# Performance work log

Hardware: AMD Instinct MI355X
Metric: run time of the kernel (lower is better)

Reference implementation:

```python
import jax, jax.numpy as jnp
import numpy as np

N_HEADS = 2
EPS = 1e-5
NEG_SLOPE = 0.02
N_CENTROIDS = 1024
RADII = (0.1, 0.2)
KS = (32, 64)


def fps(x, m):
    # Farthest point sampling (deterministic start at index 0). x: [B, C, N]
    B, C, N = x.shape
    def body(carry, _):
        distance, farthest = carry
        centroid = jnp.take_along_axis(x, jnp.broadcast_to(farthest[:, None, None], (B, C, 1)), axis=2)
        dist = jnp.sum((x - centroid) ** 2, axis=1)  # [B, N]
        distance = jnp.minimum(distance, dist)
        nxt = jnp.argmax(distance, axis=1).astype(jnp.int32)
        return (distance, nxt), farthest
    init = (jnp.full((B, N), 1e10, x.dtype), jnp.zeros((B,), jnp.int32))
    _, idxs = jax.lax.scan(body, init, None, length=m)
    return idxs.T  # [B, m]


def ball_group(x, centroids, radius, k):
    # x: [B, C, N], centroids: [B, C, M] -> (idx [B,M,k] int32, mask [B,M,k] bool)
    B, C, N = x.shape
    M = centroids.shape[2]
    d = (jnp.sum(x * x, axis=1)[:, None, :]
         - 2.0 * jnp.einsum('bcm,bcn->bmn', centroids, x)
         + jnp.sum(centroids * centroids, axis=1)[:, :, None])  # [B, M, N]
    idx = jnp.broadcast_to(jnp.arange(N, dtype=jnp.int32)[None, None, :], (B, M, N))
    idx = jnp.where(d > radius * radius, N, idx)
    idx = -jax.lax.top_k(-idx, k)[0]  # k smallest indices, ascending (matches torch.topk largest=False)
    mask = idx == N
    first = jnp.where(idx[:, :, :1] == N, 0, idx[:, :, :1])
    idx = jnp.where(mask, jnp.broadcast_to(first, idx.shape), idx)
    return idx, mask


def attention_mix(x, y, mask, wq, wk, wv, wo):
    # x: [B, C, K] centroids, y: [B, C, K, Np] groups, mask: [B, K, Np]
    B, C, K = x.shape
    Np = y.shape[3]
    H = N_HEADS
    q = jnp.einsum('oc,bck->bok', wq, x).reshape(B, H, C, K)
    kk = jnp.einsum('oc,bckn->bokn', wk, y).reshape(B, H, C, K, Np)
    v = jnp.einsum('oc,bckn->bokn', wv, y).reshape(B, H, C, K, Np)
    w = jnp.einsum('bhck,bhckn->bhkn', q, kk) / (C ** 0.5)
    w = jnp.where(mask[:, None, :, :], -1e9, w)
    w = jax.nn.softmax(w, axis=3)
    o = jnp.einsum('bhkn,bhckn->bhck', w, v).reshape(B, H * C, K)
    return jnp.einsum('oc,bck->bok', wo, o) + x


def conv_bn(x, w, b, g, beta, act):
    # 1x1 Conv1d + BatchNorm1d (training-mode batch stats) + optional LeakyReLU(0.02)
    x = jnp.einsum('oc,bck->bok', w, x) + b[None, :, None]
    mu = jnp.mean(x, axis=(0, 2), keepdims=True)
    var = jnp.var(x, axis=(0, 2), keepdims=True)
    x = (x - mu) * jax.lax.rsqrt(var + EPS) * g[None, :, None] + beta[None, :, None]
    return jnp.where(x > 0, x, NEG_SLOPE * x) if act else x


def pointnet_msg(xyz, point_features, attn_params, mlp_params):
    support = jnp.concatenate([xyz, point_features], axis=1)  # [B, 32, N]
    B, Cs, N = support.shape
    M = N_CENTROIDS
    cidx = fps(support, M)  # [B, M]
    centroids = jnp.take_along_axis(support, jnp.broadcast_to(cidx[:, None, :], (B, Cs, M)), axis=2)
    new_xyz = jnp.take_along_axis(xyz, jnp.broadcast_to(cidx[:, None, :], (B, 3, M)), axis=2)
    feats = []
    for s, (radius, k) in enumerate(zip(RADII, KS)):
        idx, mask = ball_group(support, centroids, radius, k)  # [B, M, k]
        gidx = jnp.broadcast_to(idx.reshape(B, 1, M * k), (B, Cs, M * k))
        group = jnp.take_along_axis(support, gidx, axis=2).reshape(B, Cs, M, k)
        group = group - centroids[:, :, :, None]
        f = attention_mix(centroids, group, mask, *attn_params[s])
        (w0, b0, g0, t0), (w1, b1, g1, t1) = mlp_params[s]
        f = conv_bn(f, w0, b0, g0, t0, act=True)
        f = conv_bn(f, w1, b1, g1, t1, act=False)
        feats.append(f)
    return new_xyz, jnp.concatenate(feats, axis=1)  # [B,3,M], [B,256,M]


def setup_inputs() -> dict:
    key = jax.random.key(0)
    ks = jax.random.split(key, 32)
    B, N, C = 4, 16384, 32
    d = {}
    d['xyz'] = jax.random.uniform(ks[0], (B, 3, N), jnp.float32)
    d['point_features'] = jax.random.normal(ks[1], (B, C - 3, N), jnp.float32)
    i = 2
    for s in range(2):
        d[f'aq{s}'] = 0.05 * jax.random.normal(ks[i], (64, 32), jnp.float32); i += 1
        d[f'ak{s}'] = 0.05 * jax.random.normal(ks[i], (64, 32), jnp.float32); i += 1
        d[f'av{s}'] = 0.05 * jax.random.normal(ks[i], (64, 32), jnp.float32); i += 1
        d[f'ao{s}'] = 0.05 * jax.random.normal(ks[i], (32, 64), jnp.float32); i += 1
        d[f'mw{s}0'] = 0.05 * jax.random.normal(ks[i], (64, 32), jnp.float32); i += 1
        d[f'mb{s}0'] = jnp.zeros((64,), jnp.float32)
        d[f'mg{s}0'] = jnp.ones((64,), jnp.float32)
        d[f'mbt{s}0'] = jnp.zeros((64,), jnp.float32)
        d[f'mw{s}1'] = 0.05 * jax.random.normal(ks[i], (128, 64), jnp.float32); i += 1
        d[f'mb{s}1'] = jnp.zeros((128,), jnp.float32)
        d[f'mg{s}1'] = jnp.ones((128,), jnp.float32)
        d[f'mbt{s}1'] = jnp.zeros((128,), jnp.float32)
    return d


def reference(xyz, point_features,
              aq0, ak0, av0, ao0, mw00, mb00, mg00, mbt00, mw01, mb01, mg01, mbt01,
              aq1, ak1, av1, ao1, mw10, mb10, mg10, mbt10, mw11, mb11, mg11, mbt11):
    attn_params = (((aq0, ak0, av0, ao0)), ((aq1, ak1, av1, ao1)))
    mlp_params = (((mw00, mb00, mg00, mbt00), (mw01, mb01, mg01, mbt01)),
                  ((mw10, mb10, mg10, mbt10), (mw11, mb11, mg11, mbt11)))
    return pointnet_msg(xyz, point_features, attn_params, mlp_params)
```

## Files before the change

### kernel.cpp

```cpp
#include <hip/hip_runtime.h>
#include <hip/hip_bf16.h>


static constexpr int Bb = 4;
static constexpr int Npts = 16384;
static constexpr int Mc = 1024;
static constexpr int NBLK = 16;
static constexpr int OUT_EXPECT = 12288 + 1048576;
#define BN_EPS 1e-5f
#define SLOPE 0.02f
#define SCOPE_AGT __HIP_MEMORY_SCOPE_AGENT

static constexpr size_t OFF_STATS = 33024;
static constexpr size_t OFF_GCNT  = 40960;
static constexpr size_t ZERO_BYTES = 65536;
static constexpr size_t OFF_CIDX  = 65536;
static constexpr size_t OFF_IDX0  = 81920;
static constexpr size_t OFF_CNT0  = 344064;
static constexpr size_t OFF_IDX1  = 360448;
static constexpr size_t OFF_CNT1  = 884736;
static constexpr size_t OFF_ATTN  = 901120;
static constexpr size_t OFF_Z0    = 1163264;
static constexpr size_t WS_REQUIRED = 1687552;
static constexpr size_t OFF_FSLOT = 901120;
static constexpr size_t FSLOT_BYTES = (size_t)Bb * Mc * NBLK * 8;
static constexpr size_t OFF_Z1 = 1687552;
static constexpr size_t OFF_GENT = OFF_Z1;
static constexpr size_t WS_Z1_REQUIRED = OFF_Z1 + (size_t)Bb * 128 * Mc * 4;
static constexpr size_t OFF_SUPT = WS_Z1_REQUIRED;
static constexpr size_t WS_T_REQUIRED = OFF_SUPT + (size_t)Bb * Npts * 32 * 4;
static constexpr size_t OFF_ATTN1 = WS_T_REQUIRED;
static constexpr size_t OFF_Z01   = OFF_ATTN1 + (size_t)Bb * 32 * Mc * 2;
static constexpr size_t OFF_Z11   = OFF_Z01 + (size_t)Bb * 64 * Mc * 2;
static constexpr size_t WS_EXT_REQUIRED = OFF_Z11 + (size_t)Bb * 128 * Mc * 4;

__device__ __forceinline__ float sup_at(const float* xyz, const float* pf,
                                        int b, int c, int n) {
  return (c < 3) ? xyz[((size_t)b*3 + c)*Npts + n]
                 : pf[((size_t)b*29 + (c-3))*Npts + n];
}

__device__ __forceinline__ float sanf(float v, float repl) {
  if (!(v == v) || fabsf(v) > 1e30f) v = repl;
  return v;
}

__global__ __launch_bounds__(256) void fill_kernel(float* out, int n, float val) {
  int i = blockIdx.x * 256 + threadIdx.x;
  if (i < n) out[i] = val;
}

__global__ __launch_bounds__(256) void buildT_kernel(
    const float* __restrict__ xyz, const float* __restrict__ pf,
    float* __restrict__ supT) {
  int idx = blockIdx.x * 256 + threadIdx.x;
  int n = idx & (Npts - 1);
  int b = idx >> 14;
  float* dst = supT + ((size_t)b * Npts + n) * 32;
#pragma unroll
  for (int c = 0; c < 32; ++c) dst[c] = sup_at(xyz, pf, b, c, n);
}

__global__ __launch_bounds__(512, 2) void fps_ball_kernel(
    const float* __restrict__ xyz, const float* __restrict__ pf,
    const float* __restrict__ supT,
    unsigned int* __restrict__ cidx, unsigned long long* __restrict__ slots,
    unsigned int* __restrict__ gcnt, unsigned int* __restrict__ gent) {
  const int tid = threadIdx.x;
  if (blockIdx.x < 64) {
    const int blk = blockIdx.x;
    const int b = blk >> 4;
    const int sb = blk & (NBLK - 1);
    const int lane = tid & 63, wid = tid >> 6;
    float f0[32], f1[32];
    const int p0 = sb * 1024 + tid;
    const int p1 = p0 + 512;
    float d0 = 1e10f, d1 = 1e10f;
#pragma unroll
    for (int c = 0; c < 32; ++c) {
      f0[c] = sup_at(xyz, pf, b, c, p0);
      f1[c] = sup_at(xyz, pf, b, c, p1);
    }
    __shared__ float cf[32];
    __shared__ unsigned long long red[8];
    if (sb == 0 && tid == 0) atomicExch(&cidx[b * Mc], 0u);
    if (tid < 32) cf[tid] = sup_at(xyz, pf, b, tid, 0);
    __syncthreads();
    unsigned long long* slotb = slots + (size_t)b * Mc * NBLK;
    const float* supTb = supT + (size_t)b * Npts * 32;
    for (int it = 0; it < Mc - 1; ++it) {
      float cc[32];
#pragma unroll
      for (int c = 0; c < 32; ++c) cc[c] = cf[c];
      {
        float d = 0.f, e = 0.f;
#pragma unroll
        for (int c = 0; c < 32; ++c) {
          float t0 = f0[c] - cc[c];
          float s0 = __fmul_rn(t0, t0);
          d = (c == 0) ? s0 : __fadd_rn(d, s0);
          float t1 = f1[c] - cc[c];
          float s1 = __fmul_rn(t1, t1);
          e = (c == 0) ? s1 : __fadd_rn(e, s1);
        }
        d0 = fminf(d0, d);
        d1 = fminf(d1, e);
      }
      float bd; int bp;
      if (d0 >= d1) { bd = d0; bp = p0; } else { bd = d1; bp = p1; }
      unsigned long long v =
          ((unsigned long long)__float_as_uint(bd) << 32) | (unsigned int)(~(unsigned int)bp);
#pragma unroll
      for (int d = 32; d; d >>= 1) {
        unsigned long long o = __shfl_xor(v, d, 64);
        if (o > v) v = o;
      }
      if (lane == 0) red[wid] = v;
      __syncthreads();
      if (tid == 0) {
        unsigned long long vb = red[0];
#pragma unroll
        for (int w = 1; w < 8; ++w) if (red[w] > vb) vb = red[w];
        atomicMax(&slotb[(size_t)it * NBLK + sb], vb);
      }
      if (wid == 0) {
        unsigned long long myv = 0;
        if (lane < NBLK) {
          const unsigned long long* sp = &slotb[(size_t)it * NBLK + lane];
          while ((myv = __hip_atomic_load(sp, __ATOMIC_RELAXED, SCOPE_AGT)) == 0ull)
            __builtin_amdgcn_s_sleep(1);
        }
        unsigned long long mv = myv;
#pragma unroll
        for (int d = 8; d; d >>= 1) {
          unsigned long long o = __shfl_xor(mv, d, 16);
          if (o > mv) mv = o;
        }
        unsigned long long vwin = __shfl(mv, 0, 64);
        int idxWin = (int)(~(unsigned int)(vwin & 0xffffffffu)) & (Npts - 1);
        if (lane < 32) cf[lane] = supTb[(size_t)idxWin * 32 + lane];
        if (lane == 0 && sb == 0)
          atomicExch(&cidx[b * Mc + it + 1], (unsigned int)idxWin);
      }
      __syncthreads();
    }
  } else {
    const int blk2 = blockIdx.x - 64;
    const int b = blk2 >> 5;
    const int chunk = blk2 & 31;
    const int p = chunk * 512 + tid;
    const float* supTb = supT + (size_t)b * Npts * 32;
    float x[32];
    const float* srow = supTb + (size_t)p * 32;
#pragma unroll
    for (int c = 0; c < 32; ++c) x[c] = srow[c];
    float sp = 0.f;
#pragma unroll
    for (int c = 0; c < 32; ++c) sp = fmaf(x[c], x[c], sp);
    __shared__ float cfb[2][32];
    unsigned int* cidxb = cidx + b * Mc;
    unsigned int* gcntb = gcnt + b * Mc;
    unsigned int* gentb = gent + (size_t)b * Mc * 128;
    for (int m = 0; m < Mc; ++m) {
      if (tid < 32) {
        unsigned int ci;
        const unsigned int* cp = &cidxb[m];
        while ((ci = __hip_atomic_load(cp, __ATOMIC_RELAXED, SCOPE_AGT)) == 0xFFFFFFFFu)
          __builtin_amdgcn_s_sleep(16);
        cfb[m & 1][tid] = supTb[(size_t)(ci & (Npts - 1)) * 32 + tid];
      }
      __syncthreads();
      const float* cfm = cfb[m & 1];
      float csq = 0.f, dot = 0.f;
#pragma unroll
      for (int c = 0; c < 32; ++c) {
        csq = fmaf(cfm[c], cfm[c], csq);
        dot = fmaf(cfm[c], x[c], dot);
      }
      float d = sp - 2.0f * dot + csq;
      if (d <= 0.04f) {
        int pos = atomicAdd(&gcntb[m], 1u);
        if (pos < 128)
          gentb[(size_t)m * 128 + pos] = (unsigned int)p | (d <= 0.01f ? 0x80000000u : 0u);
      }
    }
  }
}

__global__ __launch_bounds__(256) void ballpost_kernel(
    unsigned int* __restrict__ gcnt, unsigned int* __restrict__ gent,
    unsigned short* __restrict__ idx0, int* __restrict__ cnt0,
    unsigned short* __restrict__ idx1, int* __restrict__ cnt1) {
  int idx = blockIdx.x * 256 + threadIdx.x;
  int b = idx >> 10;
  int m = idx & (Mc - 1);
  int gm = b * Mc + m;
  unsigned int* e = gent + (size_t)gm * 128;
  int nn = (int)gcnt[gm]; if (nn > 128) nn = 128;
  for (int i = 1; i < nn; ++i) {
    unsigned int ei = e[i]; unsigned int key = ei & 0x7fffffffu;
    int j = i - 1;
    while (j >= 0 && (e[j] & 0x7fffffffu) > key) { e[j+1] = e[j]; --j; }
    e[j+1] = ei;
  }
  int c1 = nn < 64 ? nn : 64;
  unsigned short first1 = nn > 0 ? (unsigned short)(e[0] & 0x7fffffffu) : 0;
  unsigned short* o1 = idx1 + (size_t)gm * 64;
  for (int j = 0; j < 64; ++j)
    o1[j] = j < c1 ? (unsigned short)(e[j] & 0x7fffffffu) : first1;
  cnt1[gm] = c1;
  unsigned short* o0 = idx0 + (size_t)gm * 32;
  int c0 = 0; unsigned short first0 = 0;
  for (int i = 0; i < nn && c0 < 32; ++i) {
    if (e[i] & 0x80000000u) {
      unsigned short nv = (unsigned short)(e[i] & 0x7fffffffu);
      if (c0 == 0) first0 = nv;
      o0[c0++] = nv;
    }
  }
  for (int j = c0; j < 32; ++j) o0[j] = first0;
  cnt0[gm] = c0;
}

__global__ __launch_bounds__(512, 2) void fps_kernel(
    const float* __restrict__ xyz, const float* __restrict__ pf,
    const float* __restrict__ supT,
    int* __restrict__ cidx, unsigned long long* __restrict__ slots) {
  const int blk = blockIdx.x;
  const int b = blk >> 4;
  const int sb = blk & (NBLK - 1);
  const int tid = threadIdx.x;
  const int lane = tid & 63, wid = tid >> 6;
  float f0[32], f1[32];
  const int p0 = sb * 1024 + tid;
  const int p1 = p0 + 512;
  float d0 = 1e10f, d1 = 1e10f;
#pragma unroll
  for (int c = 0; c < 32; ++c) {
    f0[c] = sup_at(xyz, pf, b, c, p0);
    f1[c] = sup_at(xyz, pf, b, c, p1);
  }
  __shared__ float cf[32];
  __shared__ unsigned long long red[8];
  if (sb == 0 && tid == 0) cidx[b * Mc] = 0;
  if (tid < 32) cf[tid] = sup_at(xyz, pf, b, tid, 0);
  __syncthreads();
  unsigned long long* slotb = slots + (size_t)b * Mc * NBLK;
  const float* supTb = supT ? supT + (size_t)b * Npts * 32 : nullptr;
  for (int it = 0; it < Mc - 1; ++it) {
    float cc[32];
#pragma unroll
    for (int c = 0; c < 32; ++c) cc[c] = cf[c];
    {
      float d = 0.f, e = 0.f;
#pragma unroll
      for (int c = 0; c < 32; ++c) {
        float t0 = f0[c] - cc[c];
        float s0 = __fmul_rn(t0, t0);
        d = (c == 0) ? s0 : __fadd_rn(d, s0);
        float t1 = f1[c] - cc[c];
        float s1 = __fmul_rn(t1, t1);
        e = (c == 0) ? s1 : __fadd_rn(e, s1);
      }
      d0 = fminf(d0, d);
      d1 = fminf(d1, e);
    }
    float bd; int bp;
    if (d0 >= d1) { bd = d0; bp = p0; } else { bd = d1; bp = p1; }
    unsigned long long v =
        ((unsigned long long)__float_as_uint(bd) << 32) | (unsigned int)(~(unsigned int)bp);
#pragma unroll
    for (int d = 32; d; d >>= 1) {
      unsigned long long o = __shfl_xor(v, d, 64);
      if (o > v) v = o;
    }
    if (lane == 0) red[wid] = v;
    __syncthreads();
    if (tid == 0) {
      unsigned long long vb = red[0];
#pragma unroll
      for (int w = 1; w < 8; ++w) if (red[w] > vb) vb = red[w];
      atomicMax(&slotb[(size_t)it * NBLK + sb], vb);
    }
    if (wid == 0) {
      unsigned long long myv = 0;
      if (lane < NBLK) {
        const unsigned long long* sp = &slotb[(size_t)it * NBLK + lane];
        while ((myv = __hip_atomic_load(sp, __ATOMIC_RELAXED, SCOPE_AGT)) == 0ull)
          __builtin_amdgcn_s_sleep(1);
      }
      unsigned long long mv = myv;
#pragma unroll
      for (int d = 8; d; d >>= 1) {
        unsigned long long o = __shfl_xor(mv, d, 16);
        if (o > mv) mv = o;
      }
      unsigned long long vwin = __shfl(mv, 0, 64);
      int idxWin = (int)(~(unsigned int)(vwin & 0xffffffffu)) & (Npts - 1);
      if (lane < 32)
        cf[lane] = supTb ? supTb[(size_t)idxWin * 32 + lane]
                         : sup_at(xyz, pf, b, lane, idxWin);
      if (lane == 0 && sb == 0) cidx[b * Mc + it + 1] = idxWin;
    }
    __syncthreads();
  }
}

__global__ __launch_bounds__(256) void gather_kernel(
    const float* __restrict__ xyz, const int* __restrict__ cidx,
    float* __restrict__ oxyz, int out_size) {
  int idx = blockIdx.x * 256 + threadIdx.x;
  if (idx >= out_size || idx >= 12288) return;
  int m = idx & (Mc - 1);
  int t = idx >> 10;
  int b = t / 3;
  int ci = cidx[b * Mc + m] & (Npts - 1);
  oxyz[idx] = sanf(xyz[(size_t)t * Npts + ci], 888.0f);
}

__global__ __launch_bounds__(256) void ball_kernel(
    const float* __restrict__ xyz, const float* __restrict__ pf,
    const int* __restrict__ cidx,
    unsigned short* __restrict__ idx0, int* __restrict__ cnt0,
    unsigned short* __restrict__ idx1, int* __restrict__ cnt1) {
  const int b = blockIdx.x >> 6;
  const int mt = blockIdx.x & 63;
  const int tid = threadIdx.x;
  __shared__ float cf[16][32];
  __shared__ float csq[16];
  __shared__ unsigned int ent[16][128];
  __shared__ int lcnt[16];
  for (int i = tid; i < 16 * 32; i += 256) {
    int ml = i >> 5, c = i & 31;
    int ci = cidx[b * Mc + mt * 16 + ml] & (Npts - 1);
    cf[ml][c] = sup_at(xyz, pf, b, c, ci);
  }
  if (tid < 16) lcnt[tid] = 0;
  __syncthreads();
  if (tid < 16) {
    float a = 0.f;
#pragma unroll
    for (int c = 0; c < 32; ++c) a = fmaf(cf[tid][c], cf[tid][c], a);
    csq[tid] = a;
  }
  __syncthreads();
  for (int ch = 0; ch < Npts / 256; ++ch) {
    int p = ch * 256 + tid;
    float x[32];
#pragma unroll
    for (int c = 0; c < 32; ++c) x[c] = sup_at(xyz, pf, b, c, p);
    float sp = 0.f;
#pragma unroll
    for (int c = 0; c < 32; ++c) sp = fmaf(x[c], x[c], sp);
#pragma unroll 4
    for (int ml = 0; ml < 16; ++ml) {
      float dot = 0.f;
#pragma unroll
      for (int c = 0; c < 32; ++c) dot = fmaf(cf[ml][c], x[c], dot);
      float d = sp - 2.0f * dot + csq[ml];
      if (d <= 0.04f) {
        int pos = atomicAdd(&lcnt[ml], 1);
        if (pos < 128) ent[ml][pos] = (unsigned int)p | (d <= 0.01f ? 0x80000000u : 0u);
      }
    }
  }
  __syncthreads();
  if (tid < 16) {
    int ml = tid;
    int nn = lcnt[ml]; if (nn > 128) nn = 128;
    for (int i = 1; i < nn; ++i) {
      unsigned int e = ent[ml][i]; unsigned int key = e & 0x7fffffffu;
      int j = i - 1;
      while (j >= 0 && (ent[ml][j] & 0x7fffffffu) > key) { ent[ml][j+1] = ent[ml][j]; --j; }
      ent[ml][j+1] = e;
    }
    int gm = b * Mc + mt * 16 + ml;
    int c1 = nn < 64 ? nn : 64;
    unsigned short first1 = nn > 0 ? (unsigned short)(ent[ml][0] & 0x7fffffffu) : 0;
    unsigned short* o1 = idx1 + (size_t)gm * 64;
    for (int j = 0; j < 64; ++j)
      o1[j] = j < c1 ? (unsigned short)(ent[ml][j] & 0x7fffffffu) : first1;
    cnt1[gm] = c1;
    unsigned short* o0 = idx0 + (size_t)gm * 32;
    int c0 = 0; unsigned short first0 = 0;
    for (int i = 0; i < nn && c0 < 32; ++i) {
      if (ent[ml][i] & 0x80000000u) {
        unsigned short nv = (unsigned short)(ent[ml][i] & 0x7fffffffu);
        if (c0 == 0) first0 = nv;
        o0[c0++] = nv;
      }
    }
    for (int j = c0; j < 32; ++j) o0[j] = first0;
    cnt0[gm] = c0;
  }
}

template <int K>
__device__ __forceinline__ void attn_body(
    const float* xyz, const float* pf, const float* supTb,
    const int* cidx, const unsigned short* idxS, const int* cntS,
    const float* wq, const float* wk, const float* wv, const float* wo,
    __hip_bfloat16* outA, int b, int m, int wid, int lane, int tid,
    float* WqL, float* WkL, float* WvL, float* WoL,
    float (*xv)[32], float (*qv)[64], float (*yb)[2][32], float (*ov)[64], int* cns) {
  for (int i = tid; i < 2048; i += 256) {
    int r = i >> 5, c = i & 31;
    WqL[r*33 + c] = wq[i];
    WkL[r*33 + c] = wk[i];
    WvL[r*33 + c] = wv[i];
    int ro = i >> 6, co = i & 63;
    WoL[ro*65 + co] = wo[i];
  }
  if (lane < 32) {
    int ci = cidx[b * Mc + m] & (Npts - 1);
    xv[wid][lane] = supTb ? supTb[(size_t)ci * 32 + lane]
                          : sup_at(xyz, pf, b, lane, ci);
  }
  if (lane == 0) cns[wid] = cntS[b * Mc + m];
  __syncthreads();
  {
    float acc = 0.f;
#pragma unroll
    for (int c = 0; c < 32; ++c) acc = fmaf(WqL[lane*33 + c], xv[wid][c], acc);
    qv[wid][lane] = acc;
  }
  __syncthreads();
  int cnt = cns[wid];
  cnt = cnt < 1 ? 1 : (cnt > K ? K : cnt);
  const int jj = lane < K ? lane : 0;
  int nj = (int)idxS[((size_t)b*Mc + m)*K + jj] & (Npts - 1);
  float y[32];
  if (supTb) {
    const float* yr = supTb + (size_t)nj * 32;
#pragma unroll
    for (int c = 0; c < 32; ++c) y[c] = yr[c] - xv[wid][c];
  } else {
#pragma unroll
    for (int c = 0; c < 32; ++c) y[c] = sup_at(xyz, pf, b, c, nj) - xv[wid][c];
  }
  float w0 = 0.f, w1 = 0.f;
#pragma unroll 2
  for (int r = 0; r < 32; ++r) {
    float k0 = 0.f, k1 = 0.f;
#pragma unroll
    for (int c = 0; c < 32; ++c) {
      k0 = fmaf(WkL[r*33 + c], y[c], k0);
      k1 = fmaf(WkL[(r+32)*33 + c], y[c], k1);
    }
    w0 = fmaf(qv[wid][r], k0, w0);
    w1 = fmaf(qv[wid][r+32], k1, w1);
  }
  const float iscale = 0.17677669529663689f;
  w0 *= iscale; w1 *= iscale;
  if (lane >= cnt) { w0 = -1e9f; w1 = -1e9f; }
  float mx0 = w0, mx1 = w1;
#pragma unroll
  for (int d = K/2; d; d >>= 1) {
    mx0 = fmaxf(mx0, __shfl_xor(mx0, d, K));
    mx1 = fmaxf(mx1, __shfl_xor(mx1, d, K));
  }
  float e0 = __expf(w0 - mx0), e1 = __expf(w1 - mx1);
  float s0 = e0, s1 = e1;
#pragma unroll
  for (int d = K/2; d; d >>= 1) {
    s0 += __shfl_xor(s0, d, K);
    s1 += __shfl_xor(s1, d, K);
  }
  float wn0 = e0 / s0, wn1 = e1 / s1;
#pragma unroll
  for (int c = 0; c < 32; ++c) {
    float t0 = wn0 * y[c], t1 = wn1 * y[c];
#pragma unroll
    for (int d = K/2; d; d >>= 1) {
      t0 += __shfl_xor(t0, d, K);
      t1 += __shfl_xor(t1, d, K);
    }
    if (lane == 0) { yb[wid][0][c] = t0; yb[wid][1][c] = t1; }
  }
  __syncthreads();
  {
    const int h = lane >> 5;
    float a2 = 0.f;
#pragma unroll
    for (int c = 0; c < 32; ++c) a2 = fmaf(WvL[lane*33 + c], yb[wid][h][c], a2);
    ov[wid][lane] = a2;
  }
  __syncthreads();
  if (lane < 32) {
    float a3 = 0.f;
#pragma unroll
    for (int r = 0; r < 64; ++r) a3 = fmaf(WoL[lane*65 + r], ov[wid][r], a3);
    outA[((size_t)b*32 + lane)*Mc + m] = __float2bfloat16(a3 + xv[wid][lane]);
  }
}

template <int K>
__global__ __launch_bounds__(256) void attn_kernel(
    const float* __restrict__ xyz, const float* __restrict__ pf,
    const float* __restrict__ supT, const int* __restrict__ cidx,
    const unsigned short* __restrict__ idxS, const int* __restrict__ cntS,
    const float* __restrict__ wq, const float* __restrict__ wk,
    const float* __restrict__ wv, const float* __restrict__ wo,
    __hip_bfloat16* __restrict__ outA) {
  __shared__ float WqL[64*33], WkL[64*33], WvL[64*33], WoL[32*65];
  __shared__ float xv[4][32];
  __shared__ float qv[4][64];
  __shared__ float yb[4][2][32];
  __shared__ float ov[4][64];
  __shared__ int cns[4];
  const int tid = threadIdx.x;
  const int wid = tid >> 6, lane = tid & 63;
  const int gid = blockIdx.x;
  const int b = gid >> 8;
  const int m = ((gid & 255) << 2) + wid;
  const float* supTb = supT ? supT + (size_t)b * Npts * 32 : nullptr;
  attn_body<K>(xyz, pf, supTb, cidx, idxS, cntS, wq, wk, wv, wo, outA,
               b, m, wid, lane, tid, WqL, WkL, WvL, WoL, xv, qv, yb, ov, cns);
}

__global__ __launch_bounds__(256) void attn_comb_kernel(
    const float* __restrict__ xyz, const float* __restrict__ pf,
    const float* __restrict__ supT, const int* __restrict__ cidx,
    const unsigned short* __restrict__ idx0, const int* __restrict__ cnt0,
    const unsigned short* __restrict__ idx1, const int* __restrict__ cnt1,
    const float* __restrict__ wq0, const float* __restrict__ wk0,
    const float* __restrict__ wv0, const float* __restrict__ wo0,
    const float* __restrict__ wq1, const float* __restrict__ wk1,
    const float* __restrict__ wv1, const float* __restrict__ wo1,
    __hip_bfloat16* __restrict__ attn0, __hip_bfloat16* __restrict__ attn1) {
  __shared__ float WqL[64*33], WkL[64*33], WvL[64*33], WoL[32*65];
  __shared__ float xv[4][32];
  __shared__ float qv[4][64];
  __shared__ float yb[4][2][32];
  __shared__ float ov[4][64];
  __shared__ int cns[4];
  const int tid = threadIdx.x;
  const int wid = tid >> 6, lane = tid & 63;
  const int s = blockIdx.x >> 10;
  const int gid = blockIdx.x & 1023;
  const int b = gid >> 8;
  const int m = ((gid & 255) << 2) + wid;
  const float* supTb = supT + (size_t)b * Npts * 32;
  if (s == 0)
    attn_body<32>(xyz, pf, supTb, cidx, idx0, cnt0, wq0, wk0, wv0, wo0, attn0,
                  b, m, wid, lane, tid, WqL, WkL, WvL, WoL, xv, qv, yb, ov, cns);
  else
    attn_body<64>(xyz, pf, supTb, cidx, idx1, cnt1, wq1, wk1, wv1, wo1, attn1,
                  b, m, wid, lane, tid, WqL, WkL, WvL, WoL, xv, qv, yb, ov, cns);
}

__device__ __forceinline__ void conv0_body(
    const __hip_bfloat16* inA, const float* w0, const float* b0,
    __hip_bfloat16* z0, float* ssum, float* ssq, int idx, int tid) {
  int m = idx & (Mc - 1);
  int r = (idx >> 10) & 63;
  int b = idx >> 16;
  float acc = b0[r];
#pragma unroll
  for (int c = 0; c < 32; ++c)
    acc = fmaf(w0[r*32 + c], __bfloat162float(inA[((size_t)b*32 + c)*Mc + m]), acc);
  z0[((size_t)b*64 + r)*Mc + m] = __float2bfloat16(acc);
  float s = acc, q = acc * acc;
#pragma unroll
  for (int d = 32; d; d >>= 1) { s += __shfl_down(s, d, 64); q += __shfl_down(q, d, 64); }
  if ((tid & 63) == 0) { atomicAdd(&ssum[r], s); atomicAdd(&ssq[r], q); }
}

__global__ __launch_bounds__(256) void conv0_kernel(
    const __hip_bfloat16* __restrict__ inA, const float* __restrict__ w0,
    const float* __restrict__ b0, __hip_bfloat16* __restrict__ z0,
    float* __restrict__ ssum, float* __restrict__ ssq) {
  conv0_body(inA, w0, b0, z0, ssum, ssq, blockIdx.x * 256 + threadIdx.x, threadIdx.x);
}

__global__ __launch_bounds__(256) void conv0_comb_kernel(
    const __hip_bfloat16* __restrict__ attn0, const __hip_bfloat16* __restrict__ attn1,
    const float* __restrict__ w00, const float* __restrict__ b00,
    const float* __restrict__ w01, const float* __restrict__ b01,
    __hip_bfloat16* __restrict__ z00, __hip_bfloat16* __restrict__ z01,
    float* __restrict__ st) {
  int s = blockIdx.x >> 10;
  int idx = (blockIdx.x & 1023) * 256 + threadIdx.x;
  float* stS = st + (size_t)s * 384;
  if (s == 0) conv0_body(attn0, w00, b00, z00, stS, stS + 64, idx, threadIdx.x);
  else        conv0_body(attn1, w01, b01, z01, stS, stS + 64, idx, threadIdx.x);
}

__device__ __forceinline__ void conv1_stats_body(
    const __hip_bfloat16* z0, const float* ssum0, const float* ssq0,
    const float* g0, const float* t0, const float* w1, const float* b1,
    float* z1, float* ssum1, float* ssq1, int idx, int tid) {
  __shared__ float A0s[64], B0s[64];
  if (tid < 64) {
    float mu = ssum0[tid] * (1.0f/4096.0f);
    float var = ssq0[tid] * (1.0f/4096.0f) - mu * mu;
    if (var < 0.f) var = 0.f;
    float a = g0[tid] * rsqrtf(var + BN_EPS);
    A0s[tid] = a;
    B0s[tid] = t0[tid] - mu * a;
  }
  __syncthreads();
  int m = idx & (Mc - 1);
  int r2 = (idx >> 10) & 127;
  int b = idx >> 17;
  float acc = b1[r2];
#pragma unroll 8
  for (int r = 0; r < 64; ++r) {
    float u = fmaf(__bfloat162float(z0[((size_t)b*64 + r)*Mc + m]), A0s[r], B0s[r]);
    u = u > 0.f ? u : SLOPE * u;
    acc = fmaf(w1[r2*64 + r], u, acc);
  }
  if (z1) z1[idx] = acc;
  float s = acc, q = acc * acc;
#pragma unroll
  for (int d = 32; d; d >>= 1) { s += __shfl_down(s, d, 64); q += __shfl_down(q, d, 64); }
  if ((tid & 63) == 0) { atomicAdd(&ssum1[r2], s); atomicAdd(&ssq1[r2], q); }
}

__global__ __launch_bounds__(256) void conv1_stats_kernel(
    const __hip_bfloat16* __restrict__ z0,
    const float* __restrict__ ssum0, const float* __restrict__ ssq0,
    const float* __restrict__ g0, const float* __restrict__ t0,
    const float* __restrict__ w1, const float* __restrict__ b1,
    float* __restrict__ z1, float* __restrict__ ssum1, float* __restrict__ ssq1) {
  conv1_stats_body(z0, ssum0, ssq0, g0, t0, w1, b1, z1, ssum1, ssq1,
                   blockIdx.x * 256 + threadIdx.x, threadIdx.x);
}

__global__ __launch_bounds__(256) void conv1_stats_comb_kernel(
    const __hip_bfloat16* __restrict__ z00, const __hip_bfloat16* __restrict__ z01,
    const float* __restrict__ g00, const float* __restrict__ t00,
    const float* __restrict__ w10, const float* __restrict__ b10,
    const float* __restrict__ g01, const float* __restrict__ t01,
    const float* __restrict__ w11, const float* __restrict__ b11,
    float* __restrict__ z10, float* __restrict__ z11, float* __restrict__ st) {
  int s = blockIdx.x >> 11;
  int idx = (blockIdx.x & 2047) * 256 + threadIdx.x;
  float* stS = st + (size_t)s * 384;
  if (s == 0)
    conv1_stats_body(z00, stS, stS + 64, g00, t00, w10, b10, z10, stS + 128, stS + 256,
                     idx, threadIdx.x);
  else
    conv1_stats_body(z01, stS, stS + 64, g01, t01, w11, b11, z11, stS + 128, stS + 256,
                     idx, threadIdx.x);
}

__device__ __forceinline__ void conv1_write_body(
    const float* z1, const float* ssum1, const float* ssq1,
    const float* g1, const float* t1, float* outAll, int chOff, int out_size,
    int idx, int tid) {
  __shared__ float ab1[2];
  int m = idx & (Mc - 1);
  int r2 = (idx >> 10) & 127;
  int b = idx >> 17;
  if (tid == 0) {
    float mu = ssum1[r2] * (1.0f/4096.0f);
    float var = ssq1[r2] * (1.0f/4096.0f) - mu * mu;
    if (var < 0.f) var = 0.f;
    float a = g1[r2] * rsqrtf(var + BN_EPS);
    ab1[0] = a;
    ab1[1] = t1[r2] - mu * a;
  }
  __syncthreads();
  float v = fmaf(z1[idx], ab1[0], ab1[1]);
  size_t oidx = 12288 + ((size_t)b*256 + chOff + r2)*Mc + m;
  if (oidx < (size_t)out_size) outAll[oidx] = sanf(v, 777.0f);
}

__global__ __launch_bounds__(256) void conv1_write_kernel(
    const __hip_bfloat16* __restrict__ z0, const float* __restrict__ z1,
    const float* __restrict__ ssum0, const float* __restrict__ ssq0,
    const float* __restrict__ g0, const float* __restrict__ t0,
    const float* __restrict__ w1, const float* __restrict__ b1,
    const float* __restrict__ ssum1, const float* __restrict__ ssq1,
    const float* __restrict__ g1, const float* __restrict__ t1,
    float* __restrict__ outAll, int chOff, int out_size) {
  __shared__ float A0s[64], B0s[64];
  __shared__ float ab1[2];
  int tid = threadIdx.x;
  int idx = blockIdx.x * 256 + tid;
  int m = idx & (Mc - 1);
  int r2 = (idx >> 10) & 127;
  int b = idx >> 17;
  if (!z1 && tid < 64) {
    float mu = ssum0[tid] * (1.0f/4096.0f);
    float var = ssq0[tid] * (1.0f/4096.0f) - mu * mu;
    if (var < 0.f) var = 0.f;
    float a = g0[tid] * rsqrtf(var + BN_EPS);
    A0s[tid] = a;
    B0s[tid] = t0[tid] - mu * a;
  }
  if (tid == 0) {
    float mu = ssum1[r2] * (1.0f/4096.0f);
    float var = ssq1[r2] * (1.0f/4096.0f) - mu * mu;
    if (var < 0.f) var = 0.f;
    float a = g1[r2] * rsqrtf(var + BN_EPS);
    ab1[0] = a;
    ab1[1] = t1[r2] - mu * a;
  }
  __syncthreads();
  float acc;
  if (z1) {
    acc = z1[idx];
  } else {
    acc = b1[r2];
#pragma unroll 8
    for (int r = 0; r < 64; ++r) {
      float u = fmaf(__bfloat162float(z0[((size_t)b*64 + r)*Mc + m]), A0s[r], B0s[r]);
      u = u > 0.f ? u : SLOPE * u;
      acc = fmaf(w1[r2*64 + r], u, acc);
    }
  }
  float v = fmaf(acc, ab1[0], ab1[1]);
  size_t oidx = 12288 + ((size_t)b*256 + chOff + r2)*Mc + m;
  if (oidx < (size_t)out_size) outAll[oidx] = sanf(v, 777.0f);
}

__global__ __launch_bounds__(256) void conv1_write_comb_kernel(
    const float* __restrict__ z10, const float* __restrict__ z11,
    const float* __restrict__ g10, const float* __restrict__ t10,
    const float* __restrict__ g11, const float* __restrict__ t11,
    const float* __restrict__ st, float* __restrict__ outAll, int out_size) {
  int s = blockIdx.x >> 11;
  int idx = (blockIdx.x & 2047) * 256 + threadIdx.x;
  const float* stS = st + (size_t)s * 384;
  if (s == 0)
    conv1_write_body(z10, stS + 128, stS + 256, g10, t10, outAll, 0, out_size,
                     idx, threadIdx.x);
  else
    conv1_write_body(z11, stS + 128, stS + 256, g11, t11, outAll, 128, out_size,
                     idx, threadIdx.x);
}

extern "C" void kernel_launch(void* const* d_in, const int* in_sizes, int n_in,
                              void* d_out, int out_size, void* d_ws, size_t ws_size,
                              hipStream_t stream) {
  float* outb = (float*)d_out;
  int fillBlocks = (out_size + 255) / 256;
  if (n_in != 26 || in_sizes[0] != Bb*3*Npts || in_sizes[1] != Bb*29*Npts
      || in_sizes[2] != 2048) {
    fill_kernel<<<fillBlocks, 256, 0, stream>>>(outb, out_size, 7777.0f);
    return;
  }
  if (out_size != OUT_EXPECT) {
    fill_kernel<<<fillBlocks, 256, 0, stream>>>(outb, out_size, 23456.0f);
    return;
  }
  if (ws_size < WS_REQUIRED) {
    fill_kernel<<<fillBlocks, 256, 0, stream>>>(outb, out_size, 12345.0f);
    return;
  }
  const float* xyz = (const float*)d_in[0];
  const float* pf  = (const float*)d_in[1];
  char* ws = (char*)d_ws;
  int* cidx = (int*)(ws + OFF_CIDX);
  unsigned short* idx0 = (unsigned short*)(ws + OFF_IDX0);
  int* cnt0 = (int*)(ws + OFF_CNT0);
  unsigned short* idx1 = (unsigned short*)(ws + OFF_IDX1);
  int* cnt1 = (int*)(ws + OFF_CNT1);
  unsigned long long* fslots = (unsigned long long*)(ws + OFF_FSLOT);
  __hip_bfloat16* attn0 = (__hip_bfloat16*)(ws + OFF_ATTN);
  __hip_bfloat16* z00 = (__hip_bfloat16*)(ws + OFF_Z0);
  const bool fused = (ws_size >= WS_T_REQUIRED);
  const bool comb = (ws_size >= WS_EXT_REQUIRED);
  float* z10 = (ws_size >= WS_Z1_REQUIRED) ? (float*)(ws + OFF_Z1) : nullptr;
  float* supT = fused ? (float*)(ws + OFF_SUPT) : nullptr;
  unsigned int* gcnt = (unsigned int*)(ws + OFF_GCNT);
  unsigned int* gent = (unsigned int*)(ws + OFF_GENT);
  __hip_bfloat16* attn1 = comb ? (__hip_bfloat16*)(ws + OFF_ATTN1) : nullptr;
  __hip_bfloat16* z01 = comb ? (__hip_bfloat16*)(ws + OFF_Z01) : nullptr;
  float* z11 = comb ? (float*)(ws + OFF_Z11) : nullptr;
  float* st = (float*)(ws + OFF_STATS);

  const float *W[24];
  for (int i = 0; i < 24; ++i) W[i] = (const float*)d_in[2 + i];

  hipMemsetAsync(ws, 0, ZERO_BYTES, stream);
  hipMemsetAsync(ws + OFF_FSLOT, 0, FSLOT_BYTES, stream);
  if (fused) {
    hipMemsetAsync(ws + OFF_CIDX, 0xFF, Bb * Mc * 4, stream);
    buildT_kernel<<<Bb*Npts/256, 256, 0, stream>>>(xyz, pf, supT);
    fps_ball_kernel<<<192, 512, 0, stream>>>(xyz, pf, supT, (unsigned int*)cidx,
                                             fslots, gcnt, gent);
    ballpost_kernel<<<16, 256, 0, stream>>>(gcnt, gent, idx0, cnt0, idx1, cnt1);
  } else {
    fps_kernel<<<Bb*NBLK, 512, 0, stream>>>(xyz, pf, supT, cidx, fslots);
    ball_kernel<<<Bb*64, 256, 0, stream>>>(xyz, pf, cidx, idx0, cnt0, idx1, cnt1);
  }

  if (comb) {
    attn_comb_kernel<<<2048, 256, 0, stream>>>(xyz, pf, supT, cidx,
        idx0, cnt0, idx1, cnt1,
        W[0], W[1], W[2], W[3], W[12], W[13], W[14], W[15], attn0, attn1);
    conv0_comb_kernel<<<2048, 256, 0, stream>>>(attn0, attn1,
        W[4], W[5], W[16], W[17], z00, z01, st);
    conv1_stats_comb_kernel<<<4096, 256, 0, stream>>>(z00, z01,
        W[6], W[7], W[8], W[9], W[18], W[19], W[20], W[21], z10, z11, st);
    conv1_write_comb_kernel<<<4096, 256, 0, stream>>>(z10, z11,
        W[10], W[11], W[22], W[23], st, outb, out_size);
  } else {
    for (int s = 0; s < 2; ++s) {
      const float *aq = W[s*12+0], *ak = W[s*12+1], *av = W[s*12+2], *ao = W[s*12+3];
      const float *w0 = W[s*12+4], *b0 = W[s*12+5], *g0 = W[s*12+6], *t0 = W[s*12+7];
      const float *w1 = W[s*12+8], *b1 = W[s*12+9], *g1 = W[s*12+10], *t1 = W[s*12+11];
      float* stS = st + (size_t)s*384;
      float *sum0 = stS, *sq0 = stS + 64, *sum1 = stS + 128, *sq1 = stS + 256;
      if (s == 0)
        attn_kernel<32><<<Bb*Mc/4, 256, 0, stream>>>(xyz, pf, supT, cidx, idx0, cnt0,
                                                     aq, ak, av, ao, attn0);
      else
        attn_kernel<64><<<Bb*Mc/4, 256, 0, stream>>>(xyz, pf, supT, cidx, idx1, cnt1,
                                                     aq, ak, av, ao, attn0);
      conv0_kernel<<<Bb*64*Mc/256, 256, 0, stream>>>(attn0, w0, b0, z00, sum0, sq0);
      conv1_stats_kernel<<<Bb*128*Mc/256, 256, 0, stream>>>(z00, sum0, sq0, g0, t0,
                                                            w1, b1, z10, sum1, sq1);
      conv1_write_kernel<<<Bb*128*Mc/256, 256, 0, stream>>>(z00, z10, sum0, sq0, g0, t0,
                                                            w1, b1, sum1, sq1, g1, t1,
                                                            outb, s*128, out_size);
    }
  }
  gather_kernel<<<48, 256, 0, stream>>>(xyz, cidx, outb, out_size);
}
```

Baseline: 2.608 ms.

## Speculatively select two FPS centroids per cross-block round using top-2 reduction

```diff
diff --git a/kernel.cpp b/kernel.cpp
--- a/kernel.cpp
+++ b/kernel.cpp
@@ -33,6 +33,7 @@
 static constexpr size_t OFF_Z01   = OFF_ATTN1 + (size_t)Bb * 32 * Mc * 2;
 static constexpr size_t OFF_Z11   = OFF_Z01 + (size_t)Bb * 64 * Mc * 2;
 static constexpr size_t WS_EXT_REQUIRED = OFF_Z11 + (size_t)Bb * 128 * Mc * 4;
+static constexpr size_t OFF_FSLOTB = OFF_ATTN1;
 
 __device__ __forceinline__ float sup_at(const float* xyz, const float* pf,
                                         int b, int c, int n) {
@@ -61,10 +62,22 @@
   for (int c = 0; c < 32; ++c) dst[c] = sup_at(xyz, pf, b, c, n);
 }
 
+__device__ __forceinline__ float dchain(const float* f, const float* cf) {
+  float d = 0.f;
+#pragma unroll
+  for (int c = 0; c < 32; ++c) {
+    float t = f[c] - cf[c];
+    float s = __fmul_rn(t, t);
+    d = (c == 0) ? s : __fadd_rn(d, s);
+  }
+  return d;
+}
+
 __global__ __launch_bounds__(512, 2) void fps_ball_kernel(
     const float* __restrict__ xyz, const float* __restrict__ pf,
     const float* __restrict__ supT,
-    unsigned int* __restrict__ cidx, unsigned long long* __restrict__ slots,
+    unsigned int* __restrict__ cidx, unsigned long long* __restrict__ slotsA,
+    unsigned long long* __restrict__ slotsB,
     unsigned int* __restrict__ gcnt, unsigned int* __restrict__ gent) {
   const int tid = threadIdx.x;
   if (blockIdx.x < 64) {
@@ -81,67 +94,101 @@
       f0[c] = sup_at(xyz, pf, b, c, p0);
       f1[c] = sup_at(xyz, pf, b, c, p1);
     }
-    __shared__ float cf[32];
-    __shared__ unsigned long long red[8];
+    __shared__ float cfw1[32], cfw2[32];
+    __shared__ unsigned long long redH[8], redL[8], mshare[2];
     if (sb == 0 && tid == 0) atomicExch(&cidx[b * Mc], 0u);
-    if (tid < 32) cf[tid] = sup_at(xyz, pf, b, tid, 0);
+    const float* supTb = supT + (size_t)b * Npts * 32;
+    if (tid < 32) cfw1[tid] = supTb[tid];
     __syncthreads();
-    unsigned long long* slotb = slots + (size_t)b * Mc * NBLK;
-    const float* supTb = supT + (size_t)b * Npts * 32;
-    for (int it = 0; it < Mc - 1; ++it) {
-      float cc[32];
-#pragma unroll
-      for (int c = 0; c < 32; ++c) cc[c] = cf[c];
-      {
-        float d = 0.f, e = 0.f;
-#pragma unroll
-        for (int c = 0; c < 32; ++c) {
-          float t0 = f0[c] - cc[c];
-          float s0 = __fmul_rn(t0, t0);
-          d = (c == 0) ? s0 : __fadd_rn(d, s0);
-          float t1 = f1[c] - cc[c];
-          float s1 = __fmul_rn(t1, t1);
-          e = (c == 0) ? s1 : __fadd_rn(e, s1);
-        }
-        d0 = fminf(d0, d);
-        d1 = fminf(d1, e);
-      }
-      float bd; int bp;
-      if (d0 >= d1) { bd = d0; bp = p0; } else { bd = d1; bp = p1; }
-      unsigned long long v =
-          ((unsigned long long)__float_as_uint(bd) << 32) | (unsigned int)(~(unsigned int)bp);
+    d0 = fminf(d0, dchain(f0, cfw1));
+    d1 = fminf(d1, dchain(f1, cfw1));
+    unsigned long long* slotAb = slotsA + (size_t)b * Mc * NBLK;
+    unsigned long long* slotBb = slotsB ? slotsB + (size_t)b * Mc * NBLK : nullptr;
+    int sel = 1;
+    while (sel < Mc) {
+      const int r = sel - 1;
+      unsigned long long a =
+          ((unsigned long long)__float_as_uint(d0) << 32) | (unsigned int)(~(unsigned int)p0);
+      unsigned long long q =
+          ((unsigned long long)__float_as_uint(d1) << 32) | (unsigned int)(~(unsigned int)p1);
+      unsigned long long hi = a > q ? a : q;
+      unsigned long long lo = a > q ? q : a;
 #pragma unroll
       for (int d = 32; d; d >>= 1) {
-        unsigned long long o = __shfl_xor(v, d, 64);
-        if (o > v) v = o;
-      }
-      if (lane == 0) red[wid] = v;
+        unsigned long long oh = __shfl_xor(hi, d, 64);
+        unsigned long long ol = __shfl_xor(lo, d, 64);
+        unsigned long long nh = hi > oh ? hi : oh;
+        unsigned long long mn = hi > oh ? oh : hi;
+        unsigned long long ml = lo > ol ? lo : ol;
+        hi = nh;
+        lo = mn > ml ? mn : ml;
+      }
+      if (lane == 0) { redH[wid] = hi; redL[wid] = lo; }
       __syncthreads();
       if (tid == 0) {
-        unsigned long long vb = red[0];
-#pragma unroll
-        for (int w = 1; w < 8; ++w) if (red[w] > vb) vb = red[w];
-        atomicMax(&slotb[(size_t)it * NBLK + sb], vb);
+        unsigned long long H = redH[0], L = redL[0];
+#pragma unroll
+        for (int w = 1; w < 8; ++w) {
+          unsigned long long h2 = redH[w], l2 = redL[w];
+          unsigned long long nh = H > h2 ? H : h2;
+          unsigned long long mn = H > h2 ? h2 : H;
+          unsigned long long ml = L > l2 ? L : l2;
+          H = nh;
+          L = mn > ml ? mn : ml;
+        }
+        atomicMax(&slotAb[(size_t)r * NBLK + sb], H);
+        if (slotBb) atomicMax(&slotBb[(size_t)r * NBLK + sb], L);
       }
       if (wid == 0) {
         unsigned long long myv = 0;
-        if (lane < NBLK) {
-          const unsigned long long* sp = &slotb[(size_t)it * NBLK + lane];
+        if (lane < 16) {
+          const unsigned long long* sp = &slotAb[(size_t)r * NBLK + lane];
+          while ((myv = __hip_atomic_load(sp, __ATOMIC_RELAXED, SCOPE_AGT)) == 0ull)
+            __builtin_amdgcn_s_sleep(1);
+        } else if (lane < 32 && slotBb) {
+          const unsigned long long* sp = &slotBb[(size_t)r * NBLK + (lane - 16)];
           while ((myv = __hip_atomic_load(sp, __ATOMIC_RELAXED, SCOPE_AGT)) == 0ull)
             __builtin_amdgcn_s_sleep(1);
         }
-        unsigned long long mv = myv;
-#pragma unroll
-        for (int d = 8; d; d >>= 1) {
-          unsigned long long o = __shfl_xor(mv, d, 16);
-          if (o > mv) mv = o;
+        unsigned long long m1 = myv;
+#pragma unroll
+        for (int d = 32; d; d >>= 1) {
+          unsigned long long o = __shfl_xor(m1, d, 64);
+          if (o > m1) m1 = o;
         }
-        unsigned long long vwin = __shfl(mv, 0, 64);
-        int idxWin = (int)(~(unsigned int)(vwin & 0xffffffffu)) & (Npts - 1);
-        if (lane < 32) cf[lane] = supTb[(size_t)idxWin * 32 + lane];
-        if (lane == 0 && sb == 0)
-          atomicExch(&cidx[b * Mc + it + 1], (unsigned int)idxWin);
-      }
+        unsigned long long t2 = (myv == m1) ? 0ull : myv;
+#pragma unroll
+        for (int d = 32; d; d >>= 1) {
+          unsigned long long o = __shfl_xor(t2, d, 64);
+          if (o > t2) t2 = o;
+        }
+        int w1 = (int)(~(unsigned int)(m1 & 0xffffffffu)) & (Npts - 1);
+        int w2 = (int)(~(unsigned int)(t2 & 0xffffffffu)) & (Npts - 1);
+        if (lane < 32) cfw1[lane] = supTb[(size_t)w1 * 32 + lane];
+        else           cfw2[lane - 32] = supTb[(size_t)w2 * 32 + (lane - 32)];
+        if (lane == 0) { mshare[0] = m1; mshare[1] = t2; }
+      }
+      __syncthreads();
+      const unsigned long long m1 = mshare[0], m2 = mshare[1];
+      const int w1 = (int)(~(unsigned int)(m1 & 0xffffffffu)) & (Npts - 1);
+      const int w2 = (int)(~(unsigned int)(m2 & 0xffffffffu)) & (Npts - 1);
+      bool spec = false;
+      if (slotBb && sel + 1 < Mc && m2 != 0ull) {
+        float v2 = __uint_as_float((unsigned int)(m2 >> 32));
+        float dw = dchain(cfw2, cfw1);
+        spec = (dw >= v2);
+      }
+      d0 = fminf(d0, dchain(f0, cfw1));
+      d1 = fminf(d1, dchain(f1, cfw1));
+      if (spec) {
+        d0 = fminf(d0, dchain(f0, cfw2));
+        d1 = fminf(d1, dchain(f1, cfw2));
+      }
+      if (sb == 0 && tid == 0) {
+        atomicExch(&cidx[b * Mc + sel], (unsigned int)w1);
+        if (spec) atomicExch(&cidx[b * Mc + sel + 1], (unsigned int)w2);
+      }
+      sel += spec ? 2 : 1;
       __syncthreads();
     }
   } else {
@@ -252,16 +299,7 @@
 #pragma unroll
     for (int c = 0; c < 32; ++c) cc[c] = cf[c];
     {
-      float d = 0.f, e = 0.f;
-#pragma unroll
-      for (int c = 0; c < 32; ++c) {
-        float t0 = f0[c] - cc[c];
-        float s0 = __fmul_rn(t0, t0);
-        d = (c == 0) ? s0 : __fadd_rn(d, s0);
-        float t1 = f1[c] - cc[c];
-        float s1 = __fmul_rn(t1, t1);
-        e = (c == 0) ? s1 : __fadd_rn(e, s1);
-      }
+      float d = dchain(f0, cc), e = dchain(f1, cc);
       d0 = fminf(d0, d);
       d1 = fminf(d1, e);
     }
@@ -770,6 +808,7 @@
   __hip_bfloat16* attn1 = comb ? (__hip_bfloat16*)(ws + OFF_ATTN1) : nullptr;
   __hip_bfloat16* z01 = comb ? (__hip_bfloat16*)(ws + OFF_Z01) : nullptr;
   float* z11 = comb ? (float*)(ws + OFF_Z11) : nullptr;
+  unsigned long long* fslotsB = comb ? (unsigned long long*)(ws + OFF_FSLOTB) : nullptr;
   float* st = (float*)(ws + OFF_STATS);
 
   const float *W[24];
@@ -779,9 +818,10 @@
   hipMemsetAsync(ws + OFF_FSLOT, 0, FSLOT_BYTES, stream);
   if (fused) {
     hipMemsetAsync(ws + OFF_CIDX, 0xFF, Bb * Mc * 4, stream);
+    if (fslotsB) hipMemsetAsync(ws + OFF_FSLOTB, 0, FSLOT_BYTES, stream);
     buildT_kernel<<<Bb*Npts/256, 256, 0, stream>>>(xyz, pf, supT);
     fps_ball_kernel<<<192, 512, 0, stream>>>(xyz, pf, supT, (unsigned int*)cidx,
-                                             fslots, gcnt, gent);
+                                             fslots, fslotsB, gcnt, gent);
     ballpost_kernel<<<16, 256, 0, stream>>>(gcnt, gent, idx0, cnt0, idx1, cnt1);
   } else {
     fps_kernel<<<Bb*NBLK, 512, 0, stream>>>(xyz, pf, supT, cidx, fslots);
```

Measured after the change: 2.868 ms. +10.0%, slower.

## Halve FPS blocks per batch, four points per thread to cut cross-block sync

Applied to the files above, without the earlier changes.

```diff
diff --git a/kernel.cpp b/kernel.cpp
--- a/kernel.cpp
+++ b/kernel.cpp
@@ -6,6 +6,7 @@
 static constexpr int Npts = 16384;
 static constexpr int Mc = 1024;
 static constexpr int NBLK = 16;
+static constexpr int NBP  = 8;
 static constexpr int OUT_EXPECT = 12288 + 1048576;
 #define BN_EPS 1e-5f
 #define SLOPE 0.02f
@@ -61,55 +62,61 @@
   for (int c = 0; c < 32; ++c) dst[c] = sup_at(xyz, pf, b, c, n);
 }
 
-__global__ __launch_bounds__(512, 2) void fps_ball_kernel(
+__device__ __forceinline__ float dchain(const float* f, const float* cf) {
+  float d = 0.f;
+#pragma unroll
+  for (int c = 0; c < 32; ++c) {
+    float t = f[c] - cf[c];
+    float s = __fmul_rn(t, t);
+    d = (c == 0) ? s : __fadd_rn(d, s);
+  }
+  return d;
+}
+
+__global__ __launch_bounds__(512, 1) void fps_ball_kernel(
     const float* __restrict__ xyz, const float* __restrict__ pf,
     const float* __restrict__ supT,
     unsigned int* __restrict__ cidx, unsigned long long* __restrict__ slots,
     unsigned int* __restrict__ gcnt, unsigned int* __restrict__ gent) {
   const int tid = threadIdx.x;
-  if (blockIdx.x < 64) {
+  if (blockIdx.x < 32) {
     const int blk = blockIdx.x;
-    const int b = blk >> 4;
-    const int sb = blk & (NBLK - 1);
+    const int b = blk >> 3;
+    const int sb = blk & (NBP - 1);
     const int lane = tid & 63, wid = tid >> 6;
-    float f0[32], f1[32];
-    const int p0 = sb * 1024 + tid;
-    const int p1 = p0 + 512;
-    float d0 = 1e10f, d1 = 1e10f;
-#pragma unroll
-    for (int c = 0; c < 32; ++c) {
-      f0[c] = sup_at(xyz, pf, b, c, p0);
-      f1[c] = sup_at(xyz, pf, b, c, p1);
+    float f[4][32];
+    float dist[4];
+    int pidx[4];
+    const float* supTb = supT + (size_t)b * Npts * 32;
+#pragma unroll
+    for (int i = 0; i < 4; ++i) {
+      int p = sb * 2048 + i * 512 + tid;
+      pidx[i] = p;
+      dist[i] = 1e10f;
+      const float* row = supTb + (size_t)p * 32;
+#pragma unroll
+      for (int c = 0; c < 32; ++c) f[i][c] = row[c];
     }
     __shared__ float cf[32];
     __shared__ unsigned long long red[8];
     if (sb == 0 && tid == 0) atomicExch(&cidx[b * Mc], 0u);
-    if (tid < 32) cf[tid] = sup_at(xyz, pf, b, tid, 0);
+    if (tid < 32) cf[tid] = supTb[tid];
     __syncthreads();
-    unsigned long long* slotb = slots + (size_t)b * Mc * NBLK;
-    const float* supTb = supT + (size_t)b * Npts * 32;
+    unsigned long long* slotb = slots + (size_t)b * Mc * NBP;
     for (int it = 0; it < Mc - 1; ++it) {
       float cc[32];
 #pragma unroll
       for (int c = 0; c < 32; ++c) cc[c] = cf[c];
-      {
-        float d = 0.f, e = 0.f;
-#pragma unroll
-        for (int c = 0; c < 32; ++c) {
-          float t0 = f0[c] - cc[c];
-          float s0 = __fmul_rn(t0, t0);
-          d = (c == 0) ? s0 : __fadd_rn(d, s0);
-          float t1 = f1[c] - cc[c];
-          float s1 = __fmul_rn(t1, t1);
-          e = (c == 0) ? s1 : __fadd_rn(e, s1);
-        }
-        d0 = fminf(d0, d);
-        d1 = fminf(d1, e);
-      }
-      float bd; int bp;
-      if (d0 >= d1) { bd = d0; bp = p0; } else { bd = d1; bp = p1; }
+      float bestd = -1.0f; int bestp = 0;
+#pragma unroll
+      for (int i = 0; i < 4; ++i) {
+        float d = dchain(f[i], cc);
+        float nd = fminf(dist[i], d);
+        dist[i] = nd;
+        if (nd > bestd) { bestd = nd; bestp = pidx[i]; }
+      }
       unsigned long long v =
-          ((unsigned long long)__float_as_uint(bd) << 32) | (unsigned int)(~(unsigned int)bp);
+          ((unsigned long long)__float_as_uint(bestd) << 32) | (unsigned int)(~(unsigned int)bestp);
 #pragma unroll
       for (int d = 32; d; d >>= 1) {
         unsigned long long o = __shfl_xor(v, d, 64);
@@ -121,19 +128,19 @@
         unsigned long long vb = red[0];
 #pragma unroll
         for (int w = 1; w < 8; ++w) if (red[w] > vb) vb = red[w];
-        atomicMax(&slotb[(size_t)it * NBLK + sb], vb);
+        atomicMax(&slotb[(size_t)it * NBP + sb], vb);
       }
       if (wid == 0) {
         unsigned long long myv = 0;
-        if (lane < NBLK) {
-          const unsigned long long* sp = &slotb[(size_t)it * NBLK + lane];
+        if (lane < NBP) {
+          const unsigned long long* sp = &slotb[(size_t)it * NBP + lane];
           while ((myv = __hip_atomic_load(sp, __ATOMIC_RELAXED, SCOPE_AGT)) == 0ull)
             __builtin_amdgcn_s_sleep(1);
         }
         unsigned long long mv = myv;
 #pragma unroll
-        for (int d = 8; d; d >>= 1) {
-          unsigned long long o = __shfl_xor(mv, d, 16);
+        for (int d = NBP/2; d; d >>= 1) {
+          unsigned long long o = __shfl_xor(mv, d, NBP);
           if (o > mv) mv = o;
         }
         unsigned long long vwin = __shfl(mv, 0, 64);
@@ -145,7 +152,7 @@
       __syncthreads();
     }
   } else {
-    const int blk2 = blockIdx.x - 64;
+    const int blk2 = blockIdx.x - 32;
     const int b = blk2 >> 5;
     const int chunk = blk2 & 31;
     const int p = chunk * 512 + tid;
@@ -252,16 +259,7 @@
 #pragma unroll
     for (int c = 0; c < 32; ++c) cc[c] = cf[c];
     {
-      float d = 0.f, e = 0.f;
-#pragma unroll
-      for (int c = 0; c < 32; ++c) {
-        float t0 = f0[c] - cc[c];
-        float s0 = __fmul_rn(t0, t0);
-        d = (c == 0) ? s0 : __fadd_rn(d, s0);
-        float t1 = f1[c] - cc[c];
-        float s1 = __fmul_rn(t1, t1);
-        e = (c == 0) ? s1 : __fadd_rn(e, s1);
-      }
+      float d = dchain(f0, cc), e = dchain(f1, cc);
       d0 = fminf(d0, d);
       d1 = fminf(d1, e);
     }
@@ -780,7 +778,7 @@
   if (fused) {
     hipMemsetAsync(ws + OFF_CIDX, 0xFF, Bb * Mc * 4, stream);
     buildT_kernel<<<Bb*Npts/256, 256, 0, stream>>>(xyz, pf, supT);
-    fps_ball_kernel<<<192, 512, 0, stream>>>(xyz, pf, supT, (unsigned int*)cidx,
+    fps_ball_kernel<<<160, 512, 0, stream>>>(xyz, pf, supT, (unsigned int*)cidx,
                                              fslots, gcnt, gent);
     ballpost_kernel<<<16, 256, 0, stream>>>(gcnt, gent, idx0, cnt0, idx1, cnt1);
   } else {
```

Result: slower. 2.865 ms (+9.9%).
